# Kernel optimization log

Measured on AMD Instinct MI355X. Metric: run time of the kernel, lower is better.

## Reference

```python
import jax, jax.numpy as jnp
import numpy as np

COMPRESS_RATE = 128
HEAD_DIM = 128
ROPE_DIM = 64
ROPE_THETA = 10000.0
EPS = 1e-6


def setup_inputs() -> dict:
    key = jax.random.key(0)
    ks = jax.random.split(key, 5)
    B, S, H = 2, 8192, 2048
    return {
        "hidden_states": jax.random.normal(ks[0], (B, S, H), jnp.float32),
        "q_residual": jax.random.normal(ks[1], (B, S, H), jnp.float32),
        "position_ids": jnp.broadcast_to(jnp.arange(S, dtype=jnp.int32), (B, S)),
        "w_kv": jax.random.normal(ks[2], (H, HEAD_DIM), jnp.float32) * 0.02,
        "w_gate": jax.random.normal(ks[3], (H, HEAD_DIM), jnp.float32) * 0.02,
        "position_bias": jax.random.normal(ks[4], (COMPRESS_RATE, HEAD_DIM), jnp.float32) * 0.02,
        "kv_norm_weight": jnp.ones((HEAD_DIM,), jnp.float32),
    }


def _rms_norm(x, w, eps=EPS):
    xf = x.astype(jnp.float32)
    var = jnp.mean(jnp.square(xf), axis=-1, keepdims=True)
    return (xf * jax.lax.rsqrt(var + eps)).astype(x.dtype) * w


def _rotate_half(x):
    x1, x2 = jnp.split(x, 2, axis=-1)
    return jnp.concatenate([-x2, x1], axis=-1)


def reference(hidden_states, q_residual, position_ids, w_kv, w_gate, position_bias, kv_norm_weight):
    # Stateless single-shot HCA compression (past_key_values is None):
    # compress every full window of COMPRESS_RATE tokens, drop the remainder.
    B, S, H = hidden_states.shape
    m, d = COMPRESS_RATE, HEAD_DIM
    T = S // m
    usable = T * m
    h = hidden_states[:, :usable]
    # eq. 20/21: C = H @ W_kv, Z = H @ W_gate
    kv = (h @ w_kv).reshape(B, T, m, d)      # [B,T,m,d]
    gate = (h @ w_gate).reshape(B, T, m, d)  # [B,T,m,d]
    # eq. 22: per-channel softmax over the window dim with position bias B
    w = jax.nn.softmax(gate + position_bias, axis=2)
    compressed = jnp.sum(w * kv, axis=2)     # [B,T,d]
    compressed = _rms_norm(compressed, kv_norm_weight)
    compressed = compressed[:, None]         # [B,1,T,d] single shared KV head
    # Interleaved RoPE at deterministic positions i * compress_rate (first_window_position = 0)
    half = ROPE_DIM // 2
    inv_freq = 1.0 / (ROPE_THETA ** (jnp.arange(half, dtype=jnp.float32) / half))
    pos = jnp.arange(T, dtype=jnp.float32) * m            # [T]
    freqs = pos[:, None] * inv_freq[None, :]              # [T, half]
    cos = jnp.repeat(jnp.cos(freqs), 2, axis=-1)[None, None]  # [1,1,T,ROPE_DIM]
    sin = jnp.repeat(jnp.sin(freqs), 2, axis=-1)[None, None]
    nope, rope = compressed[..., :-ROPE_DIM], compressed[..., -ROPE_DIM:]
    rotated = rope * cos + _rotate_half(rope) * sin
    return jnp.concatenate([nope, rotated], axis=-1)      # [B,1,T,d]
```

## Files before the change

### kernel.cpp

```cpp
#include <hip/hip_runtime.h>
#include <hip/hip_bf16.h>

#define HDIM 2048
#define DDIM 128
#define NT 256
#define BM 64
#define BK 32
#define LDK 40
#define MT 16384
#define TCH 64

typedef __attribute__((ext_vector_type(8))) short bf16x8_t;
typedef __attribute__((ext_vector_type(4))) float f32x4_t;

__global__ void k_detect(const unsigned short* __restrict__ h, int* __restrict__ flag) {
  int bad = 0;
  for (int i = threadIdx.x; i < 8192; i += 256) {
    int e = (h[i] >> 7) & 0xFF;
    bad |= (e >= 167) ? 1 : 0;
  }
  __shared__ int s;
  if (threadIdx.x == 0) s = 0;
  __syncthreads();
  if (bad) atomicOr(&s, 1);
  __syncthreads();
  if (threadIdx.x == 0) *flag = s;
}

__global__ void k_prep(const void* __restrict__ w_kv, const void* __restrict__ w_gate,
                       const int* __restrict__ flag, __hip_bfloat16* __restrict__ Wt) {
  __shared__ float tile[64][65];
  const int isF32 = *flag;
  const void* src = blockIdx.z ? w_gate : w_kv;
  const int k0 = blockIdx.x * 64;
  const int n0 = blockIdx.y * 64;
  const int tx = threadIdx.x & 63;
  const int ty = threadIdx.x >> 6;
#pragma unroll
  for (int i = 0; i < 16; ++i) {
    int r = i * 4 + ty;
    int idx = (k0 + r) * DDIM + n0 + tx;
    float v = isF32 ? ((const float*)src)[idx]
                    : __bfloat162float(((const __hip_bfloat16*)src)[idx]);
    tile[tx][r] = v;
  }
  __syncthreads();
#pragma unroll
  for (int i = 0; i < 16; ++i) {
    int r = i * 4 + ty;
    Wt[(blockIdx.z * DDIM + n0 + r) * HDIM + k0 + tx] = __float2bfloat16(tile[r][tx]);
  }
}

__global__ __launch_bounds__(256)
void k_gemm(const void* __restrict__ hidden, const __hip_bfloat16* __restrict__ Wt,
            const int* __restrict__ flag, __hip_bfloat16* __restrict__ C) {
  __shared__ __align__(16) __hip_bfloat16 As[BM * LDK];
  const int isF32 = *flag;
  const int tid  = threadIdx.x;
  const int bm0  = blockIdx.x * BM;
  const int wave = tid >> 6;
  const int lane = tid & 63;
  const int wn   = wave * 64;
  const int lrow = lane & 15;
  const int quad = lane >> 4;

  f32x4_t acc[4][4];
#pragma unroll
  for (int i = 0; i < 4; ++i)
#pragma unroll
    for (int j = 0; j < 4; ++j) acc[i][j] = (f32x4_t){0.f, 0.f, 0.f, 0.f};

  const int srow = tid >> 2;
  const int skg  = (tid & 3) * 8;
  const float*          Af = (const float*)hidden + (size_t)(bm0 + srow) * HDIM + skg;
  const unsigned short* Ab = (const unsigned short*)hidden + (size_t)(bm0 + srow) * HDIM + skg;

  float4 pa0, pa1;
  int4   pb;
  if (isF32) { pa0 = *(const float4*)(Af); pa1 = *(const float4*)(Af + 4); }
  else       { pb = *(const int4*)(Ab); }

  for (int k0 = 0; k0 < HDIM; k0 += BK) {
    __syncthreads();
    if (isF32) {
      union { int4 v; __hip_bfloat16 h[8]; } u;
      u.h[0] = __float2bfloat16(pa0.x); u.h[1] = __float2bfloat16(pa0.y);
      u.h[2] = __float2bfloat16(pa0.z); u.h[3] = __float2bfloat16(pa0.w);
      u.h[4] = __float2bfloat16(pa1.x); u.h[5] = __float2bfloat16(pa1.y);
      u.h[6] = __float2bfloat16(pa1.z); u.h[7] = __float2bfloat16(pa1.w);
      *(int4*)(As + srow * LDK + skg) = u.v;
    } else {
      *(int4*)(As + srow * LDK + skg) = pb;
    }
    __syncthreads();

    if (k0 + BK < HDIM) {
      if (isF32) { pa0 = *(const float4*)(Af + k0 + BK); pa1 = *(const float4*)(Af + k0 + BK + 4); }
      else       { pb = *(const int4*)(Ab + k0 + BK); }
    }

    bf16x8_t bfrag[4], afrag[4];
#pragma unroll
    for (int nt = 0; nt < 4; ++nt)
      bfrag[nt] = *(const bf16x8_t*)(Wt + (size_t)(wn + nt * 16 + lrow) * HDIM + k0 + quad * 8);
#pragma unroll
    for (int mt = 0; mt < 4; ++mt)
      afrag[mt] = *(const bf16x8_t*)(As + (mt * 16 + lrow) * LDK + quad * 8);
#pragma unroll
    for (int mt = 0; mt < 4; ++mt)
#pragma unroll
      for (int nt = 0; nt < 4; ++nt)
        acc[mt][nt] = __builtin_amdgcn_mfma_f32_16x16x32_bf16(afrag[mt], bfrag[nt], acc[mt][nt], 0, 0, 0);
  }

#pragma unroll
  for (int mt = 0; mt < 4; ++mt) {
    const int mrow = bm0 + mt * 16 + quad * 4;
#pragma unroll
    for (int nt = 0; nt < 4; ++nt) {
      const int ncol = wn + nt * 16 + lrow;
#pragma unroll
      for (int r = 0; r < 4; ++r)
        C[(size_t)(mrow + r) * NT + ncol] = __float2bfloat16(acc[mt][nt][r]);
    }
  }
}

__global__ void k_compress(const __hip_bfloat16* __restrict__ C,
                           const void* __restrict__ pbias,
                           const void* __restrict__ nw,
                           const int* __restrict__ flag,
                           void* __restrict__ out) {
  const int isF32 = *flag;
  const int j  = threadIdx.x;
  const int bt = blockIdx.x;
  const int t  = bt & (TCH - 1);
  const long i0 = (long)bt * 128;

  float mx = -3.0e38f, l = 0.f, acc = 0.f;
  for (int r = 0; r < 128; ++r) {
    const __hip_bfloat16* row = C + (i0 + r) * NT;
    float pb = isF32 ? ((const float*)pbias)[r * DDIM + j]
                     : __bfloat162float(((const __hip_bfloat16*)pbias)[r * DDIM + j]);
    float g = __bfloat162float(row[DDIM + j]) + pb;
    float v = __bfloat162float(row[j]);
    float nm = fmaxf(mx, g);
    float sc = __expf(mx - nm);
    float e  = __expf(g - nm);
    l   = l * sc + e;
    acc = acc * sc + e * v;
    mx  = nm;
  }
  float comp = acc / l;

  float sq = comp * comp;
#pragma unroll
  for (int off = 32; off > 0; off >>= 1) sq += __shfl_down(sq, off, 64);
  __shared__ float ssum[2];
  __shared__ float sh[DDIM];
  if ((j & 63) == 0) ssum[j >> 6] = sq;
  __syncthreads();
  float var = (ssum[0] + ssum[1]) * (1.0f / DDIM);
  float wv = isF32 ? ((const float*)nw)[j] : __bfloat162float(((const __hip_bfloat16*)nw)[j]);
  float y = comp * rsqrtf(var + 1e-6f) * wv;
  sh[j] = y;
  __syncthreads();

  float outv = y;
  if (j >= 64) {
    int jj = j - 64;
    int fi = jj >> 1;
    double invf = exp((double)fi * (-0.28782313662425575));
    double ang  = (double)(t * 128) * invf;
    float c = (float)cos(ang);
    float s = (float)sin(ang);
    float other = (jj < 32) ? -sh[64 + jj + 32] : sh[64 + jj - 32];
    outv = y * c + other * s;
  }
  if (isF32) ((float*)out)[bt * DDIM + j] = outv;
  else       ((__hip_bfloat16*)out)[bt * DDIM + j] = __float2bfloat16(outv);
}

extern "C" void kernel_launch(void* const* d_in, const int* in_sizes, int n_in,
                              void* d_out, int out_size, void* d_ws, size_t ws_size,
                              hipStream_t stream) {
  const void* hidden = d_in[0];
  const void* w_kv   = d_in[3];
  const void* w_gate = d_in[4];
  const void* pbias  = d_in[5];
  const void* nw     = d_in[6];

  int* flag = (int*)d_ws;
  __hip_bfloat16* Wt = (__hip_bfloat16*)((char*)d_ws + 256);
  __hip_bfloat16* C  = (__hip_bfloat16*)((char*)d_ws + 256 + (size_t)NT * HDIM * sizeof(__hip_bfloat16));

  k_detect<<<1, 256, 0, stream>>>((const unsigned short*)hidden, flag);
  k_prep<<<dim3(HDIM / 64, DDIM / 64, 2), 256, 0, stream>>>(w_kv, w_gate, flag, Wt);
  k_gemm<<<dim3(MT / BM), 256, 0, stream>>>(hidden, Wt, flag, C);
  k_compress<<<dim3(128), DDIM, 0, stream>>>(C, pbias, nw, flag, d_out);
}
```

Baseline: 340.0 us.

## Fuse dtype detection into weight prep, retile GEMM, split compress softmax across groups

Removes the separate single-block detect kernel by having every prep block redo the dtype check, which saves one launch. The GEMM moves to 32-row blocks with a 128-wide K step, doubling the grid to 512 blocks and cutting barrier count per K. The compress kernel now uses 512 threads, each group of 128 handling a quarter of the window with an online softmax whose partial states are merged through shared memory. This adds parallelism to a serial 128-step loop at the cost of extra sync and redundant detection work in each prep block.

```diff
diff --git a/kernel.cpp b/kernel.cpp
--- a/kernel.cpp
+++ b/kernel.cpp
@@ -4,33 +4,30 @@
 #define HDIM 2048
 #define DDIM 128
 #define NT 256
-#define BM 64
-#define BK 32
-#define LDK 40
+#define BM 32
+#define BK 128
+#define LDK 136
 #define MT 16384
-#define TCH 64
 
 typedef __attribute__((ext_vector_type(8))) short bf16x8_t;
 typedef __attribute__((ext_vector_type(4))) float f32x4_t;
 
-__global__ void k_detect(const unsigned short* __restrict__ h, int* __restrict__ flag) {
+__global__ void k_prep(const void* __restrict__ w_kv, const void* __restrict__ w_gate,
+                       const unsigned short* __restrict__ hidden,
+                       int* __restrict__ flag, __hip_bfloat16* __restrict__ Wt) {
+  __shared__ int sflag;
+  __shared__ float tile[64][65];
   int bad = 0;
-  for (int i = threadIdx.x; i < 8192; i += 256) {
-    int e = (h[i] >> 7) & 0xFF;
-    bad |= (e >= 167) ? 1 : 0;
-  }
-  __shared__ int s;
-  if (threadIdx.x == 0) s = 0;
-  __syncthreads();
-  if (bad) atomicOr(&s, 1);
-  __syncthreads();
-  if (threadIdx.x == 0) *flag = s;
-}
-
-__global__ void k_prep(const void* __restrict__ w_kv, const void* __restrict__ w_gate,
-                       const int* __restrict__ flag, __hip_bfloat16* __restrict__ Wt) {
-  __shared__ float tile[64][65];
-  const int isF32 = *flag;
+  for (int i = threadIdx.x; i < 8192; i += 256)
+    bad |= (((hidden[i] >> 7) & 0xFF) >= 167) ? 1 : 0;
+  if (threadIdx.x == 0) sflag = 0;
+  __syncthreads();
+  if (bad) atomicOr(&sflag, 1);
+  __syncthreads();
+  const int isF32 = sflag;
+  if (threadIdx.x == 0 && blockIdx.x == 0 && blockIdx.y == 0 && blockIdx.z == 0)
+    *flag = isF32;
+
   const void* src = blockIdx.z ? w_gate : w_kv;
   const int k0 = blockIdx.x * 64;
   const int n0 = blockIdx.y * 64;
@@ -65,57 +62,75 @@
   const int lrow = lane & 15;
   const int quad = lane >> 4;
 
-  f32x4_t acc[4][4];
-#pragma unroll
-  for (int i = 0; i < 4; ++i)
+  f32x4_t acc[2][4];
+#pragma unroll
+  for (int i = 0; i < 2; ++i)
 #pragma unroll
     for (int j = 0; j < 4; ++j) acc[i][j] = (f32x4_t){0.f, 0.f, 0.f, 0.f};
 
-  const int srow = tid >> 2;
-  const int skg  = (tid & 3) * 8;
+  const int srow = tid >> 3;
+  const int skg  = (tid & 7) * 16;
   const float*          Af = (const float*)hidden + (size_t)(bm0 + srow) * HDIM + skg;
   const unsigned short* Ab = (const unsigned short*)hidden + (size_t)(bm0 + srow) * HDIM + skg;
 
-  float4 pa0, pa1;
-  int4   pb;
-  if (isF32) { pa0 = *(const float4*)(Af); pa1 = *(const float4*)(Af + 4); }
-  else       { pb = *(const int4*)(Ab); }
+  float4 pa[4];
+  int4   pb[2];
+  if (isF32) {
+#pragma unroll
+    for (int l = 0; l < 4; ++l) pa[l] = *(const float4*)(Af + 4 * l);
+  } else {
+#pragma unroll
+    for (int l = 0; l < 2; ++l) pb[l] = *(const int4*)(Ab + 8 * l);
+  }
 
   for (int k0 = 0; k0 < HDIM; k0 += BK) {
     __syncthreads();
     if (isF32) {
-      union { int4 v; __hip_bfloat16 h[8]; } u;
-      u.h[0] = __float2bfloat16(pa0.x); u.h[1] = __float2bfloat16(pa0.y);
-      u.h[2] = __float2bfloat16(pa0.z); u.h[3] = __float2bfloat16(pa0.w);
-      u.h[4] = __float2bfloat16(pa1.x); u.h[5] = __float2bfloat16(pa1.y);
-      u.h[6] = __float2bfloat16(pa1.z); u.h[7] = __float2bfloat16(pa1.w);
-      *(int4*)(As + srow * LDK + skg) = u.v;
+#pragma unroll
+      for (int l = 0; l < 2; ++l) {
+        union { int4 v; __hip_bfloat16 h[8]; } u;
+        u.h[0] = __float2bfloat16(pa[2*l].x);   u.h[1] = __float2bfloat16(pa[2*l].y);
+        u.h[2] = __float2bfloat16(pa[2*l].z);   u.h[3] = __float2bfloat16(pa[2*l].w);
+        u.h[4] = __float2bfloat16(pa[2*l+1].x); u.h[5] = __float2bfloat16(pa[2*l+1].y);
+        u.h[6] = __float2bfloat16(pa[2*l+1].z); u.h[7] = __float2bfloat16(pa[2*l+1].w);
+        *(int4*)(As + srow * LDK + skg + 8 * l) = u.v;
+      }
     } else {
-      *(int4*)(As + srow * LDK + skg) = pb;
+#pragma unroll
+      for (int l = 0; l < 2; ++l)
+        *(int4*)(As + srow * LDK + skg + 8 * l) = pb[l];
     }
     __syncthreads();
 
     if (k0 + BK < HDIM) {
-      if (isF32) { pa0 = *(const float4*)(Af + k0 + BK); pa1 = *(const float4*)(Af + k0 + BK + 4); }
-      else       { pb = *(const int4*)(Ab + k0 + BK); }
-    }
-
-    bf16x8_t bfrag[4], afrag[4];
-#pragma unroll
-    for (int nt = 0; nt < 4; ++nt)
-      bfrag[nt] = *(const bf16x8_t*)(Wt + (size_t)(wn + nt * 16 + lrow) * HDIM + k0 + quad * 8);
-#pragma unroll
-    for (int mt = 0; mt < 4; ++mt)
-      afrag[mt] = *(const bf16x8_t*)(As + (mt * 16 + lrow) * LDK + quad * 8);
-#pragma unroll
-    for (int mt = 0; mt < 4; ++mt)
+      if (isF32) {
+#pragma unroll
+        for (int l = 0; l < 4; ++l) pa[l] = *(const float4*)(Af + k0 + BK + 4 * l);
+      } else {
+#pragma unroll
+        for (int l = 0; l < 2; ++l) pb[l] = *(const int4*)(Ab + k0 + BK + 8 * l);
+      }
+    }
+
+#pragma unroll
+    for (int kk = 0; kk < BK; kk += 32) {
+      bf16x8_t afrag[2], bfrag[4];
 #pragma unroll
       for (int nt = 0; nt < 4; ++nt)
-        acc[mt][nt] = __builtin_amdgcn_mfma_f32_16x16x32_bf16(afrag[mt], bfrag[nt], acc[mt][nt], 0, 0, 0);
-  }
-
-#pragma unroll
-  for (int mt = 0; mt < 4; ++mt) {
+        bfrag[nt] = *(const bf16x8_t*)(Wt + (size_t)(wn + nt * 16 + lrow) * HDIM + k0 + kk + quad * 8);
+#pragma unroll
+      for (int mt = 0; mt < 2; ++mt)
+        afrag[mt] = *(const bf16x8_t*)(As + (mt * 16 + lrow) * LDK + kk + quad * 8);
+#pragma unroll
+      for (int mt = 0; mt < 2; ++mt)
+#pragma unroll
+        for (int nt = 0; nt < 4; ++nt)
+          acc[mt][nt] = __builtin_amdgcn_mfma_f32_16x16x32_bf16(afrag[mt], bfrag[nt], acc[mt][nt], 0, 0, 0);
+    }
+  }
+
+#pragma unroll
+  for (int mt = 0; mt < 2; ++mt) {
     const int mrow = bm0 + mt * 16 + quad * 4;
 #pragma unroll
     for (int nt = 0; nt < 4; ++nt) {
@@ -127,59 +142,85 @@
   }
 }
 
-__global__ void k_compress(const __hip_bfloat16* __restrict__ C,
-                           const void* __restrict__ pbias,
-                           const void* __restrict__ nw,
-                           const int* __restrict__ flag,
-                           void* __restrict__ out) {
+__global__ __launch_bounds__(512)
+void k_compress(const __hip_bfloat16* __restrict__ C,
+                const void* __restrict__ pbias,
+                const void* __restrict__ nw,
+                const int* __restrict__ flag,
+                void* __restrict__ out) {
   const int isF32 = *flag;
-  const int j  = threadIdx.x;
+  const int tid = threadIdx.x;
+  const int j = tid & (DDIM - 1);
+  const int g = tid >> 7;
   const int bt = blockIdx.x;
-  const int t  = bt & (TCH - 1);
+  const int t  = bt & 63;
   const long i0 = (long)bt * 128;
 
   float mx = -3.0e38f, l = 0.f, acc = 0.f;
-  for (int r = 0; r < 128; ++r) {
+#pragma unroll 8
+  for (int rr = 0; rr < 32; ++rr) {
+    const int r = g * 32 + rr;
     const __hip_bfloat16* row = C + (i0 + r) * NT;
     float pb = isF32 ? ((const float*)pbias)[r * DDIM + j]
                      : __bfloat162float(((const __hip_bfloat16*)pbias)[r * DDIM + j]);
-    float g = __bfloat162float(row[DDIM + j]) + pb;
-    float v = __bfloat162float(row[j]);
-    float nm = fmaxf(mx, g);
+    float gt = __bfloat162float(row[DDIM + j]) + pb;
+    float v  = __bfloat162float(row[j]);
+    float nm = fmaxf(mx, gt);
     float sc = __expf(mx - nm);
-    float e  = __expf(g - nm);
+    float e  = __expf(gt - nm);
     l   = l * sc + e;
     acc = acc * sc + e * v;
     mx  = nm;
   }
-  float comp = acc / l;
-
-  float sq = comp * comp;
-#pragma unroll
-  for (int off = 32; off > 0; off >>= 1) sq += __shfl_down(sq, off, 64);
+
+  __shared__ float smx[4][DDIM], sl[4][DDIM], sa[4][DDIM];
+  __shared__ float sh[DDIM];
   __shared__ float ssum[2];
-  __shared__ float sh[DDIM];
-  if ((j & 63) == 0) ssum[j >> 6] = sq;
-  __syncthreads();
-  float var = (ssum[0] + ssum[1]) * (1.0f / DDIM);
-  float wv = isF32 ? ((const float*)nw)[j] : __bfloat162float(((const __hip_bfloat16*)nw)[j]);
-  float y = comp * rsqrtf(var + 1e-6f) * wv;
-  sh[j] = y;
-  __syncthreads();
-
-  float outv = y;
-  if (j >= 64) {
-    int jj = j - 64;
-    int fi = jj >> 1;
-    double invf = exp((double)fi * (-0.28782313662425575));
-    double ang  = (double)(t * 128) * invf;
-    float c = (float)cos(ang);
-    float s = (float)sin(ang);
-    float other = (jj < 32) ? -sh[64 + jj + 32] : sh[64 + jj - 32];
-    outv = y * c + other * s;
-  }
-  if (isF32) ((float*)out)[bt * DDIM + j] = outv;
-  else       ((__hip_bfloat16*)out)[bt * DDIM + j] = __float2bfloat16(outv);
+  smx[g][j] = mx; sl[g][j] = l; sa[g][j] = acc;
+  __syncthreads();
+
+  float comp = 0.f;
+  if (g == 0) {
+    float M = fmaxf(fmaxf(smx[0][j], smx[1][j]), fmaxf(smx[2][j], smx[3][j]));
+    float L = 0.f, A = 0.f;
+#pragma unroll
+    for (int q = 0; q < 4; ++q) {
+      float s = __expf(smx[q][j] - M);
+      L += sl[q][j] * s;
+      A += sa[q][j] * s;
+    }
+    comp = A / L;
+    float sq = comp * comp;
+#pragma unroll
+    for (int off = 32; off > 0; off >>= 1) sq += __shfl_down(sq, off, 64);
+    if ((j & 63) == 0) ssum[j >> 6] = sq;
+  }
+  __syncthreads();
+
+  if (g == 0) {
+    float var = (ssum[0] + ssum[1]) * (1.0f / DDIM);
+    float wv = isF32 ? ((const float*)nw)[j] : __bfloat162float(((const __hip_bfloat16*)nw)[j]);
+    float y = comp * rsqrtf(var + 1e-6f) * wv;
+    sh[j] = y;
+  }
+  __syncthreads();
+
+  if (g == 0) {
+    float y = sh[j];
+    float outv = y;
+    if (j >= 64) {
+      int jj = j - 64;
+      int fi = jj >> 1;
+      double invf = exp((double)fi * (-0.28782313662425575));
+      double ang  = (double)(t * 128) * invf;
+      float c = (float)cos(ang);
+      float s = (float)sin(ang);
+      float other = (jj < 32) ? -sh[64 + jj + 32] : sh[64 + jj - 32];
+      outv = y * c + other * s;
+    }
+    if (isF32) ((float*)out)[bt * DDIM + j] = outv;
+    else       ((__hip_bfloat16*)out)[bt * DDIM + j] = __float2bfloat16(outv);
+  }
 }
 
 extern "C" void kernel_launch(void* const* d_in, const int* in_sizes, int n_in,
@@ -195,8 +236,8 @@
   __hip_bfloat16* Wt = (__hip_bfloat16*)((char*)d_ws + 256);
   __hip_bfloat16* C  = (__hip_bfloat16*)((char*)d_ws + 256 + (size_t)NT * HDIM * sizeof(__hip_bfloat16));
 
-  k_detect<<<1, 256, 0, stream>>>((const unsigned short*)hidden, flag);
-  k_prep<<<dim3(HDIM / 64, DDIM / 64, 2), 256, 0, stream>>>(w_kv, w_gate, flag, Wt);
+  k_prep<<<dim3(HDIM / 64, DDIM / 64, 2), 256, 0, stream>>>(w_kv, w_gate,
+                                                            (const unsigned short*)hidden, flag, Wt);
   k_gemm<<<dim3(MT / BM), 256, 0, stream>>>(hidden, Wt, flag, C);
-  k_compress<<<dim3(128), DDIM, 0, stream>>>(C, pbias, nw, flag, d_out);
-}
+  k_compress<<<dim3(128), 512, 0, stream>>>(C, pbias, nw, flag, d_out);
+}
```

Measured after the change: 322.0 us. 5.3% less time.
